# Optimization experiments

Hardware: AMD Instinct MI355X
Metric: run time of the kernel (lower is better)

The kernel has to match this reference:

```python
import jax, jax.numpy as jnp
import numpy as np

B, N, F_IN, F_OUT = 8, 4096, 256, 256


def setup_inputs() -> dict:
    key = jax.random.key(0)
    k1, k2, k3 = jax.random.split(key, 3)
    H = jax.random.normal(k1, (B, N, F_IN), dtype=jnp.float32)
    W = jax.random.normal(k2, (F_IN, F_OUT), dtype=jnp.float32) * (1.0 / np.sqrt(F_IN))
    A = jax.random.normal(k3, (N, N), dtype=jnp.float32) * (1.414 * np.sqrt(2.0 / (N + N)))
    return {"H": H, "W": W, "A": A}


def reference(H, W, A):
    # HW: [B, N, F_out]
    HW = jnp.einsum('bnf,fo->bno', H, W)
    # symmetrize + relu -> nonneg adjacency [N, N]
    A_norm = jax.nn.relu((A + A.T) * 0.5)
    # degree and inverse sqrt (inf -> 0 for isolated nodes)
    D = jnp.sum(A_norm, axis=1)
    D_safe = jnp.where(D > 0, D, 1.0)
    d_inv_sqrt = jnp.where(D > 0, D_safe ** -0.5, 0.0)
    # L_norm = I - D^{-1/2} A D^{-1/2}  (diagonal scaling, no dense diag matmul)
    DAD = d_inv_sqrt[:, None] * A_norm * d_inv_sqrt[None, :]
    L_norm = jnp.eye(N, dtype=H.dtype) - DAD
    # output = relu(L_norm @ HW): [B, N, F_out]
    out = jnp.einsum('nm,bmo->bno', L_norm, HW)
    return jax.nn.relu(out)
```

## Files before the change

### kernel.cpp

```cpp
#include <hip/hip_runtime.h>
#include <stdint.h>

#define N_NODES 4096
#define F_DIM   256
#define BATCH   8

typedef __attribute__((ext_vector_type(8))) __bf16 bf16x8;
typedef __attribute__((ext_vector_type(4))) float  f32x4;
typedef __attribute__((ext_vector_type(8))) unsigned short u16x8;

typedef const __attribute__((address_space(1))) void* gas1_t;
typedef __attribute__((address_space(3))) void*       las3_t;

__device__ __forceinline__ void stage16(const void* g, void* l) {
  __builtin_amdgcn_global_load_lds((gas1_t)g, (las3_t)l, 16, 0, 0);
}

__device__ __forceinline__ unsigned short f2bf(float f) {
  union { float f; uint32_t u; } v; v.f = f;
  uint32_t u = v.u;
  return (unsigned short)((u + 0x7FFFu + ((u >> 16) & 1u)) >> 16);
}
__device__ __forceinline__ float bf2f(unsigned short u) {
  union { uint32_t u; float f; } v; v.u = ((uint32_t)u) << 16;
  return v.f;
}

__global__ __launch_bounds__(256) void k_pre(const float* __restrict__ A,
                                             unsigned short* __restrict__ Sb,
                                             float* __restrict__ D,
                                             const float4* __restrict__ H4,
                                             ushort4* __restrict__ Hb4,
                                             const float* __restrict__ W,
                                             unsigned short* __restrict__ Wt) {
  int t = threadIdx.x;
  int bid = blockIdx.y * 64 + blockIdx.x;
  {
    int i = bid * 512 + t;
    float4 v = H4[i];
    ushort4 o; o.x = f2bf(v.x); o.y = f2bf(v.y); o.z = f2bf(v.z); o.w = f2bf(v.w);
    Hb4[i] = o;
    i += 256;
    v = H4[i];
    o.x = f2bf(v.x); o.y = f2bf(v.y); o.z = f2bf(v.z); o.w = f2bf(v.w);
    Hb4[i] = o;
  }
  if (bid < 256) Wt[t * 256 + bid] = f2bf(W[bid * 256 + t]);

  int bi = blockIdx.y, bj = blockIdx.x;
  if (bj < bi) return;

  __shared__ __align__(16) float T1[64][68];
  __shared__ float Tt[64][67];
  __shared__ float Pr4[64][4];
  __shared__ float Pc[4][64];
  int i0 = bi * 64, j0 = bj * 64;

#pragma unroll
  for (int it = 0; it < 4; ++it) {
    int idx = it * 256 + t;
    int r = idx >> 4, c4 = (idx & 15) * 4;
    float4 v1 = *(const float4*)(A + (size_t)(i0 + r) * N_NODES + j0 + c4);
    *(float4*)&T1[r][c4] = v1;
    float4 v2 = *(const float4*)(A + (size_t)(j0 + r) * N_NODES + i0 + c4);
    Tt[c4 + 0][r] = v2.x; Tt[c4 + 1][r] = v2.y; Tt[c4 + 2][r] = v2.z; Tt[c4 + 3][r] = v2.w;
  }
  __syncthreads();

  {
    int r = t >> 2, cb = (t & 3) * 8;
    float rowpart = 0.f;
#pragma unroll
    for (int g = 0; g < 2; ++g) {
      int c0 = cb + g * 32;
      u16x8 u;
      float vv[8];
#pragma unroll
      for (int i = 0; i < 8; ++i) {
        float v = 0.5f * (T1[r][c0 + i] + Tt[r][c0 + i]);
        v = v > 0.f ? v : 0.f;
        vv[i] = v;
        rowpart += v;
        u[i] = f2bf(v);
      }
      *(u16x8*)&Sb[(size_t)(i0 + r) * N_NODES + j0 + c0] = u;
      *(float4*)&T1[r][c0]     = make_float4(vv[0], vv[1], vv[2], vv[3]);
      *(float4*)&T1[r][c0 + 4] = make_float4(vv[4], vv[5], vv[6], vv[7]);
    }
    Pr4[r][t & 3] = rowpart;
  }
  __syncthreads();

  {
    int c = t & 63, seg = t >> 6;
    float s = 0.f;
#pragma unroll
    for (int i = 0; i < 16; ++i) s += T1[seg * 16 + i][c];
    Pc[seg][c] = s;
  }
  __syncthreads();

  if (t < 64) {
    atomicAdd(&D[i0 + t], Pr4[t][0] + Pr4[t][1] + Pr4[t][2] + Pr4[t][3]);
  } else if (t < 128 && bi != bj) {
    int c = t - 64;
    atomicAdd(&D[j0 + c], Pc[0][c] + Pc[1][c] + Pc[2][c] + Pc[3][c]);
  }

  if (bi != bj) {
#pragma unroll
    for (int it = 0; it < 2; ++it) {
      int u = it * 256 + t;
      int co = u >> 3, rc = (u & 7) * 8;
      u16x8 o;
#pragma unroll
      for (int i = 0; i < 8; ++i) o[i] = f2bf(T1[rc + i][co]);
      *(u16x8*)&Sb[(size_t)(j0 + co) * N_NODES + i0 + rc] = o;
    }
  }
}

__global__ void k_dinv(const float* __restrict__ D, float* __restrict__ dinv) {
  int i = blockIdx.x * blockDim.x + threadIdx.x;
  if (i < N_NODES) {
    float d = D[i];
    dinv[i] = d > 0.f ? 1.0f / sqrtf(d) : 0.f;
  }
}

__global__ __launch_bounds__(512) void k_gemm1(const unsigned short* __restrict__ Hb,
                                               const unsigned short* __restrict__ Wt,
                                               const float* __restrict__ dinv,
                                               unsigned short* __restrict__ HWb,
                                               unsigned short* __restrict__ Gt) {
  __shared__ __align__(16) unsigned short L[65536];
  int t = threadIdx.x;
  int lane = t & 63, r16 = lane & 15, q = lane >> 4;
  int wave = t >> 6;
  int wm = wave >> 2, wn = wave & 3;
  int nh = blockIdx.x;
  int m0 = blockIdx.y * 128;
  int n0 = nh * 128;

#pragma unroll
  for (int i = 0; i < 8; ++i) {
    int s = i * 512 + t;
    int row = s >> 5, cl = s & 31;
    int cs = cl ^ (row & 7);
    uint32_t dst = (uint32_t)(i * 512 + (t & ~63)) * 16;
    stage16(Hb + (size_t)(m0 + row) * 256 + cs * 8, (char*)L + dst);
    stage16(Wt + (size_t)(n0 + row) * 256 + cs * 8, (char*)L + 65536 + dst);
  }
  __syncthreads();

  f32x4 acc[4][2];
#pragma unroll
  for (int i = 0; i < 4; ++i)
#pragma unroll
    for (int j = 0; j < 2; ++j) acc[i][j] = f32x4{0.f, 0.f, 0.f, 0.f};

#pragma unroll
  for (int ks = 0; ks < 8; ++ks) {
    bf16x8 a[4], b[2];
#pragma unroll
    for (int mi = 0; mi < 4; ++mi) {
      int ra = wm * 64 + mi * 16 + r16;
      a[mi] = *(const bf16x8*)((const char*)L + ra * 512 + (((ks * 4 + q) ^ (ra & 7)) << 4));
    }
#pragma unroll
    for (int ni = 0; ni < 2; ++ni) {
      int rb = wn * 32 + ni * 16 + r16;
      b[ni] = *(const bf16x8*)((const char*)L + 65536 + rb * 512 + (((ks * 4 + q) ^ (rb & 7)) << 4));
    }
#pragma unroll
    for (int mi = 0; mi < 4; ++mi)
#pragma unroll
      for (int ni = 0; ni < 2; ++ni)
        acc[mi][ni] = __builtin_amdgcn_mfma_f32_16x16x32_bf16(a[mi], b[ni], acc[mi][ni], 0, 0, 0);
  }
  __syncthreads();

  unsigned short (*T)[136] = (unsigned short (*)[136])L;
#pragma unroll
  for (int mi = 0; mi < 4; ++mi) {
    int rowl = wm * 64 + mi * 16 + q * 4;
#pragma unroll
    for (int ni = 0; ni < 2; ++ni) {
      int coll = wn * 32 + ni * 16 + r16;
#pragma unroll
      for (int rr = 0; rr < 4; ++rr) {
        unsigned short h = f2bf(acc[mi][ni][rr]);
        HWb[(size_t)(m0 + rowl + rr) * F_DIM + (n0 + coll)] = h;
        T[coll][rowl + rr] = h;
      }
    }
  }
  __syncthreads();

  int b = m0 >> 12, nb = m0 & 4095;
#pragma unroll
  for (int i = 0; i < 4; ++i) {
    int u = i * 512 + t;
    int co = u >> 4, cs = (u & 15) * 8;
    u16x8 v = *(const u16x8*)&T[co][cs];
    float4 d0 = *(const float4*)&dinv[nb + cs];
    float4 d1 = *(const float4*)&dinv[nb + cs + 4];
    u16x8 w;
    w[0] = f2bf(bf2f(v[0]) * d0.x);
    w[1] = f2bf(bf2f(v[1]) * d0.y);
    w[2] = f2bf(bf2f(v[2]) * d0.z);
    w[3] = f2bf(bf2f(v[3]) * d0.w);
    w[4] = f2bf(bf2f(v[4]) * d1.x);
    w[5] = f2bf(bf2f(v[5]) * d1.y);
    w[6] = f2bf(bf2f(v[6]) * d1.z);
    w[7] = f2bf(bf2f(v[7]) * d1.w);
    *(u16x8*)&Gt[(size_t)(b * 256 + n0 + co) * N_NODES + nb + cs] = w;
  }
}

#define LDSB 49152

__global__ __launch_bounds__(512, 2) void k_gemm2(const unsigned short* __restrict__ Sb,
                                                  const unsigned short* __restrict__ Gt,
                                                  const unsigned short* __restrict__ HWb,
                                                  const float* __restrict__ dinv,
                                                  float* __restrict__ Out) {
  __shared__ __align__(16) unsigned short LDS[3 * 24576];
  const int NT = N_NODES / 64;
  int t = threadIdx.x;
  int lane = t & 63, r16 = lane & 15, q = lane >> 4;
  int wave = t >> 6;
  int wm = wave >> 1, wn = wave & 1;

  int bid = blockIdx.x;
  int xcd = bid & 7, j = bid >> 3;
  int mt = (xcd >> 1) * 4 + (j & 3);
  int nt = (xcd & 1) * 8 + (j >> 2);
  int m0 = mt * 256, n0 = nt * 128;

  const char* aSrc[4]; const char* bSrc[2];
  uint32_t aDst[4], bDst[2];
#pragma unroll
  for (int i = 0; i < 4; ++i) {
    int slot = i * 512 + t;
    int row = slot >> 3;
    int c = (slot & 7) ^ (row & 7);
    aSrc[i] = (const char*)Sb + (size_t)(m0 + row) * 8192 + c * 16;
    aDst[i] = (uint32_t)(i * 512 + (t & ~63)) * 16;
  }
#pragma unroll
  for (int i = 0; i < 2; ++i) {
    int slot = i * 512 + t;
    int row = slot >> 3;
    int c = (slot & 7) ^ (row & 7);
    bSrc[i] = (const char*)Gt + (size_t)(n0 + row) * 8192 + c * 16;
    bDst[i] = 32768u + (uint32_t)(i * 512 + (t & ~63)) * 16;
  }

  int aoff[4][2], boff[4][2];
#pragma unroll
  for (int mi = 0; mi < 4; ++mi) {
    int ra = wm * 64 + mi * 16 + r16;
#pragma unroll
    for (int ks = 0; ks < 2; ++ks)
      aoff[mi][ks] = ra * 128 + (((ks * 4 + q) ^ (ra & 7)) << 4);
  }
#pragma unroll
  for (int ni = 0; ni < 4; ++ni) {
    int rb = wn * 64 + ni * 16 + r16;
#pragma unroll
    for (int ks = 0; ks < 2; ++ks)
      boff[ni][ks] = 32768 + rb * 128 + (((ks * 4 + q) ^ (rb & 7)) << 4);
  }

  f32x4 acc[4][4];
#pragma unroll
  for (int i = 0; i < 4; ++i)
#pragma unroll
    for (int jj = 0; jj < 4; ++jj) acc[i][jj] = f32x4{0.f, 0.f, 0.f, 0.f};

  auto stage_tile = [&](int kt2, uint32_t bufByte) {
    size_t kb = (size_t)kt2 * 128;
#pragma unroll
    for (int i = 0; i < 4; ++i)
      stage16(aSrc[i] + kb, (char*)LDS + bufByte + aDst[i]);
#pragma unroll
    for (int i = 0; i < 2; ++i)
      stage16(bSrc[i] + kb, (char*)LDS + bufByte + bDst[i]);
  };

  auto tile_body = [&](int kt, uint32_t cur, int mode) {
    bf16x8 aR[4][2], bR[4][2];
#pragma unroll
    for (int mi = 0; mi < 4; ++mi)
#pragma unroll
      for (int ks = 0; ks < 2; ++ks)
        aR[mi][ks] = *(const bf16x8*)((const char*)LDS + cur + aoff[mi][ks]);
#pragma unroll
    for (int ni = 0; ni < 4; ++ni)
#pragma unroll
      for (int ks = 0; ks < 2; ++ks)
        bR[ni][ks] = *(const bf16x8*)((const char*)LDS + cur + boff[ni][ks]);
    if (mode == 2) {
      uint32_t stg = cur + 2 * LDSB;
      if (stg >= 3 * LDSB) stg -= 3 * LDSB;
      stage_tile(kt + 2, stg);
    }
    __builtin_amdgcn_sched_barrier(0);
    __builtin_amdgcn_s_setprio(1);
#pragma unroll
    for (int ks = 0; ks < 2; ++ks)
#pragma unroll
      for (int mi = 0; mi < 4; ++mi)
#pragma unroll
        for (int ni = 0; ni < 4; ++ni)
          acc[mi][ni] = __builtin_amdgcn_mfma_f32_16x16x32_bf16(aR[mi][ks], bR[ni][ks], acc[mi][ni], 0, 0, 0);
    __builtin_amdgcn_s_setprio(0);
    if (mode == 2) {
      asm volatile("s_waitcnt vmcnt(6)" ::: "memory");
    } else if (mode == 1) {
      asm volatile("s_waitcnt vmcnt(0)" ::: "memory");
    }
    if (mode != 0) {
      __builtin_amdgcn_s_barrier();
      __builtin_amdgcn_sched_barrier(0);
    }
  };

  stage_tile(0, 0);
  stage_tile(1, LDSB);
  asm volatile("s_waitcnt vmcnt(6)" ::: "memory");
  __builtin_amdgcn_s_barrier();
  __builtin_amdgcn_sched_barrier(0);

  uint32_t cur = 0;
#pragma unroll 1
  for (int kt = 0; kt < NT - 2; ++kt) {
    tile_body(kt, cur, 2);
    cur += LDSB; if (cur == 3 * LDSB) cur = 0;
  }
  tile_body(NT - 2, cur, 1);
  cur += LDSB; if (cur == 3 * LDSB) cur = 0;
  tile_body(NT - 1, cur, 0);

  int bq = n0 >> 8;
#pragma unroll
  for (int mi = 0; mi < 4; ++mi) {
    int row = m0 + wm * 64 + mi * 16 + q * 4;
    float di[4];
#pragma unroll
    for (int rr = 0; rr < 4; ++rr) di[rr] = dinv[row + rr];
#pragma unroll
    for (int ni = 0; ni < 4; ++ni) {
      int col = n0 + wn * 64 + ni * 16 + r16;
      int o = col & 255;
#pragma unroll
      for (int rr = 0; rr < 4; ++rr) {
        size_t oi = ((size_t)bq * N_NODES + (row + rr)) * F_DIM + o;
        float u = bf2f(HWb[oi]) - di[rr] * acc[mi][ni][rr];
        Out[oi] = u > 0.f ? u : 0.f;
      }
    }
  }
}

extern "C" void kernel_launch(void* const* d_in, const int* in_sizes, int n_in,
                              void* d_out, int out_size, void* d_ws, size_t ws_size,
                              hipStream_t stream) {
  (void)in_sizes; (void)n_in; (void)out_size; (void)ws_size;
  const float* H = (const float*)d_in[0];
  const float* W = (const float*)d_in[1];
  const float* A = (const float*)d_in[2];
  float* out = (float*)d_out;

  char* ws = (char*)d_ws;
  size_t off = 0;
  auto alloc = [&](size_t bytes) {
    char* p = ws + off;
    off += (bytes + 255) & ~(size_t)255;
    return p;
  };
  float*          Dd   = (float*)alloc((size_t)N_NODES * 4);
  float*          dinv = (float*)alloc((size_t)N_NODES * 4);
  unsigned short* Sb   = (unsigned short*)alloc((size_t)N_NODES * N_NODES * 2);
  unsigned short* HWb  = (unsigned short*)alloc((size_t)BATCH * N_NODES * F_DIM * 2);
  unsigned short* Gt   = (unsigned short*)alloc((size_t)BATCH * F_DIM * N_NODES * 2);
  unsigned short* Wt   = (unsigned short*)alloc((size_t)F_DIM * F_DIM * 2);
  unsigned short* Hb   = (unsigned short*)alloc((size_t)BATCH * N_NODES * F_DIM * 2);

  hipMemsetAsync(Dd, 0, N_NODES * 4, stream);
  k_pre<<<dim3(64, 64), 256, 0, stream>>>(A, Sb, Dd, (const float4*)H, (ushort4*)Hb, W, Wt);
  k_dinv<<<16, 256, 0, stream>>>(Dd, dinv);
  k_gemm1<<<dim3(2, 256), 512, 0, stream>>>(Hb, Wt, dinv, HWb, Gt);
  k_gemm2<<<dim3(256), 512, 0, stream>>>(Sb, Gt, HWb, dinv, out);
}
```

Measured before the change: 220.1 us.

## Pre-swizzle Gt into MFMA fragment layout and load B directly to registers

```diff
diff --git a/kernel.cpp b/kernel.cpp
--- a/kernel.cpp
+++ b/kernel.cpp
@@ -24,6 +24,9 @@
 __device__ __forceinline__ float bf2f(unsigned short u) {
   union { uint32_t u; float f; } v; v.u = ((uint32_t)u) << 16;
   return v.f;
+}
+__device__ __forceinline__ float dinv_of(float d) {
+  return d > 0.f ? 1.0f / sqrtf(d) : 0.f;
 }
 
 __global__ __launch_bounds__(256) void k_pre(const float* __restrict__ A,
@@ -67,28 +70,35 @@
   }
   __syncthreads();
 
-  {
-    int r = t >> 2, cb = (t & 3) * 8;
-    float rowpart = 0.f;
-#pragma unroll
-    for (int g = 0; g < 2; ++g) {
-      int c0 = cb + g * 32;
-      u16x8 u;
-      float vv[8];
-#pragma unroll
-      for (int i = 0; i < 8; ++i) {
-        float v = 0.5f * (T1[r][c0 + i] + Tt[r][c0 + i]);
-        v = v > 0.f ? v : 0.f;
-        vv[i] = v;
-        rowpart += v;
-        u[i] = f2bf(v);
-      }
-      *(u16x8*)&Sb[(size_t)(i0 + r) * N_NODES + j0 + c0] = u;
-      *(float4*)&T1[r][c0]     = make_float4(vv[0], vv[1], vv[2], vv[3]);
-      *(float4*)&T1[r][c0 + 4] = make_float4(vv[4], vv[5], vv[6], vv[7]);
-    }
-    Pr4[r][t & 3] = rowpart;
-  }
+  int r = t >> 2, cb = (t & 3) * 8;
+  float vv[16];
+  float rowpart = 0.f;
+#pragma unroll
+  for (int g = 0; g < 2; ++g) {
+    int c0 = cb + g * 32;
+#pragma unroll
+    for (int i = 0; i < 8; ++i) {
+      float v = 0.5f * (T1[r][c0 + i] + Tt[r][c0 + i]);
+      v = v > 0.f ? v : 0.f;
+      vv[g * 8 + i] = v;
+      rowpart += v;
+    }
+  }
+  __syncthreads();
+
+#pragma unroll
+  for (int g = 0; g < 2; ++g) {
+    int c0 = cb + g * 32;
+    u16x8 u;
+#pragma unroll
+    for (int i = 0; i < 8; ++i) u[i] = f2bf(vv[g * 8 + i]);
+    *(u16x8*)&Sb[(size_t)(i0 + r) * N_NODES + j0 + c0] = u;
+    *(float4*)&T1[r][c0]     = make_float4(vv[g*8+0], vv[g*8+1], vv[g*8+2], vv[g*8+3]);
+    *(float4*)&T1[r][c0 + 4] = make_float4(vv[g*8+4], vv[g*8+5], vv[g*8+6], vv[g*8+7]);
+#pragma unroll
+    for (int i = 0; i < 8; ++i) Tt[c0 + i][r] = vv[g * 8 + i];
+  }
+  Pr4[r][t & 3] = rowpart;
   __syncthreads();
 
   {
@@ -114,25 +124,17 @@
       int co = u >> 3, rc = (u & 7) * 8;
       u16x8 o;
 #pragma unroll
-      for (int i = 0; i < 8; ++i) o[i] = f2bf(T1[rc + i][co]);
+      for (int i = 0; i < 8; ++i) o[i] = f2bf(Tt[co][rc + i]);
       *(u16x8*)&Sb[(size_t)(j0 + co) * N_NODES + i0 + rc] = o;
     }
-  }
-}
-
-__global__ void k_dinv(const float* __restrict__ D, float* __restrict__ dinv) {
-  int i = blockIdx.x * blockDim.x + threadIdx.x;
-  if (i < N_NODES) {
-    float d = D[i];
-    dinv[i] = d > 0.f ? 1.0f / sqrtf(d) : 0.f;
   }
 }
 
 __global__ __launch_bounds__(512) void k_gemm1(const unsigned short* __restrict__ Hb,
                                                const unsigned short* __restrict__ Wt,
-                                               const float* __restrict__ dinv,
+                                               const float* __restrict__ D,
                                                unsigned short* __restrict__ HWb,
-                                               unsigned short* __restrict__ Gt) {
+                                               unsigned short* __restrict__ Gt2) {
   __shared__ __align__(16) unsigned short L[65536];
   int t = threadIdx.x;
   int lane = t & 63, r16 = lane & 15, q = lane >> 4;
@@ -203,30 +205,32 @@
     int u = i * 512 + t;
     int co = u >> 4, cs = (u & 15) * 8;
     u16x8 v = *(const u16x8*)&T[co][cs];
-    float4 d0 = *(const float4*)&dinv[nb + cs];
-    float4 d1 = *(const float4*)&dinv[nb + cs + 4];
+    float4 d0 = *(const float4*)&D[nb + cs];
+    float4 d1 = *(const float4*)&D[nb + cs + 4];
     u16x8 w;
-    w[0] = f2bf(bf2f(v[0]) * d0.x);
-    w[1] = f2bf(bf2f(v[1]) * d0.y);
-    w[2] = f2bf(bf2f(v[2]) * d0.z);
-    w[3] = f2bf(bf2f(v[3]) * d0.w);
-    w[4] = f2bf(bf2f(v[4]) * d1.x);
-    w[5] = f2bf(bf2f(v[5]) * d1.y);
-    w[6] = f2bf(bf2f(v[6]) * d1.z);
-    w[7] = f2bf(bf2f(v[7]) * d1.w);
-    *(u16x8*)&Gt[(size_t)(b * 256 + n0 + co) * N_NODES + nb + cs] = w;
-  }
-}
-
-#define LDSB 49152
+    w[0] = f2bf(bf2f(v[0]) * dinv_of(d0.x));
+    w[1] = f2bf(bf2f(v[1]) * dinv_of(d0.y));
+    w[2] = f2bf(bf2f(v[2]) * dinv_of(d0.z));
+    w[3] = f2bf(bf2f(v[3]) * dinv_of(d0.w));
+    w[4] = f2bf(bf2f(v[4]) * dinv_of(d1.x));
+    w[5] = f2bf(bf2f(v[5]) * dinv_of(d1.y));
+    w[6] = f2bf(bf2f(v[6]) * dinv_of(d1.z));
+    w[7] = f2bf(bf2f(v[7]) * dinv_of(d1.w));
+    int r_g = b * 256 + n0 + co;
+    int k   = nb + cs;
+    int rbg = r_g >> 4, rl = r_g & 15;
+    int ktv = k >> 6, ksv = (k >> 5) & 1, qv = (k >> 3) & 3;
+    size_t addr = ((((size_t)rbg * 64 + ktv) * 2 + ksv) * 64 + (qv * 16 + rl)) * 16;
+    *(u16x8*)((char*)Gt2 + addr) = w;
+  }
+}
 
 __global__ __launch_bounds__(512, 2) void k_gemm2(const unsigned short* __restrict__ Sb,
-                                                  const unsigned short* __restrict__ Gt,
+                                                  const unsigned short* __restrict__ Gt2,
                                                   const unsigned short* __restrict__ HWb,
-                                                  const float* __restrict__ dinv,
+                                                  const float* __restrict__ D,
                                                   float* __restrict__ Out) {
-  __shared__ __align__(16) unsigned short LDS[3 * 24576];
-  const int NT = N_NODES / 64;
+  __shared__ __align__(16) unsigned short LDS[3 * 16384];
   int t = threadIdx.x;
   int lane = t & 63, r16 = lane & 15, q = lane >> 4;
   int wave = t >> 6;
@@ -238,8 +242,8 @@
   int nt = (xcd & 1) * 8 + (j >> 2);
   int m0 = mt * 256, n0 = nt * 128;
 
-  const char* aSrc[4]; const char* bSrc[2];
-  uint32_t aDst[4], bDst[2];
+  const char* aSrc[4];
+  uint32_t aDst[4];
 #pragma unroll
   for (int i = 0; i < 4; ++i) {
     int slot = i * 512 + t;
@@ -248,16 +252,8 @@
     aSrc[i] = (const char*)Sb + (size_t)(m0 + row) * 8192 + c * 16;
     aDst[i] = (uint32_t)(i * 512 + (t & ~63)) * 16;
   }
-#pragma unroll
-  for (int i = 0; i < 2; ++i) {
-    int slot = i * 512 + t;
-    int row = slot >> 3;
-    int c = (slot & 7) ^ (row & 7);
-    bSrc[i] = (const char*)Gt + (size_t)(n0 + row) * 8192 + c * 16;
-    bDst[i] = 32768u + (uint32_t)(i * 512 + (t & ~63)) * 16;
-  }
-
-  int aoff[4][2], boff[4][2];
+
+  int aoff[4][2];
 #pragma unroll
   for (int mi = 0; mi < 4; ++mi) {
     int ra = wm * 64 + mi * 16 + r16;
@@ -265,12 +261,12 @@
     for (int ks = 0; ks < 2; ++ks)
       aoff[mi][ks] = ra * 128 + (((ks * 4 + q) ^ (ra & 7)) << 4);
   }
+
+  const char* bbase[4];
 #pragma unroll
   for (int ni = 0; ni < 4; ++ni) {
-    int rb = wn * 64 + ni * 16 + r16;
-#pragma unroll
-    for (int ks = 0; ks < 2; ++ks)
-      boff[ni][ks] = 32768 + rb * 128 + (((ks * 4 + q) ^ (rb & 7)) << 4);
+    int rbg = nt * 8 + wn * 4 + ni;
+    bbase[ni] = (const char*)Gt2 + (size_t)rbg * 131072 + lane * 16;
   }
 
   f32x4 acc[4][4];
@@ -278,35 +274,36 @@
   for (int i = 0; i < 4; ++i)
 #pragma unroll
     for (int jj = 0; jj < 4; ++jj) acc[i][jj] = f32x4{0.f, 0.f, 0.f, 0.f};
+
+  bf16x8 B0[4][2], B1[4][2];
 
   auto stage_tile = [&](int kt2, uint32_t bufByte) {
     size_t kb = (size_t)kt2 * 128;
 #pragma unroll
     for (int i = 0; i < 4; ++i)
       stage16(aSrc[i] + kb, (char*)LDS + bufByte + aDst[i]);
-#pragma unroll
-    for (int i = 0; i < 2; ++i)
-      stage16(bSrc[i] + kb, (char*)LDS + bufByte + bDst[i]);
   };
 
-  auto tile_body = [&](int kt, uint32_t cur, int mode) {
-    bf16x8 aR[4][2], bR[4][2];
+  auto body = [&](int kt, uint32_t cur, bf16x8 (&Bu)[4][2], bf16x8 (&Bl)[4][2], int mode) {
+    bf16x8 aR[4][2];
 #pragma unroll
     for (int mi = 0; mi < 4; ++mi)
 #pragma unroll
       for (int ks = 0; ks < 2; ++ks)
         aR[mi][ks] = *(const bf16x8*)((const char*)LDS + cur + aoff[mi][ks]);
-#pragma unroll
-    for (int ni = 0; ni < 4; ++ni)
-#pragma unroll
-      for (int ks = 0; ks < 2; ++ks)
-        bR[ni][ks] = *(const bf16x8*)((const char*)LDS + cur + boff[ni][ks]);
+    if (mode != 0) {
+      size_t ko = (size_t)(kt + 1) * 2048;
+#pragma unroll
+      for (int ni = 0; ni < 4; ++ni)
+#pragma unroll
+        for (int ks = 0; ks < 2; ++ks)
+          Bl[ni][ks] = *(const bf16x8*)(bbase[ni] + ko + ks * 1024);
+    }
     if (mode == 2) {
-      uint32_t stg = cur + 2 * LDSB;
-      if (stg >= 3 * LDSB) stg -= 3 * LDSB;
+      uint32_t stg = cur + 65536;
+      if (stg >= 98304) stg -= 98304;
       stage_tile(kt + 2, stg);
     }
-    __builtin_amdgcn_sched_barrier(0);
     __builtin_amdgcn_s_setprio(1);
 #pragma unroll
     for (int ks = 0; ks < 2; ++ks)
@@ -314,34 +311,41 @@
       for (int mi = 0; mi < 4; ++mi)
 #pragma unroll
         for (int ni = 0; ni < 4; ++ni)
-          acc[mi][ni] = __builtin_amdgcn_mfma_f32_16x16x32_bf16(aR[mi][ks], bR[ni][ks], acc[mi][ni], 0, 0, 0);
+          acc[mi][ni] = __builtin_amdgcn_mfma_f32_16x16x32_bf16(aR[mi][ks], Bu[ni][ks], acc[mi][ni], 0, 0, 0);
     __builtin_amdgcn_s_setprio(0);
     if (mode == 2) {
-      asm volatile("s_waitcnt vmcnt(6)" ::: "memory");
-    } else if (mode == 1) {
-      asm volatile("s_waitcnt vmcnt(0)" ::: "memory");
-    }
-    if (mode != 0) {
+      asm volatile("s_waitcnt vmcnt(12)" ::: "memory");
       __builtin_amdgcn_s_barrier();
       __builtin_amdgcn_sched_barrier(0);
+    } else if (mode == 1) {
+      asm volatile("s_waitcnt vmcnt(8)" ::: "memory");
+      __builtin_amdgcn_s_barrier();
+      __builtin_amdgcn_sched_barrier(0);
     }
   };
 
+#pragma unroll
+  for (int ni = 0; ni < 4; ++ni)
+#pragma unroll
+    for (int ks = 0; ks < 2; ++ks)
+      B0[ni][ks] = *(const bf16x8*)(bbase[ni] + ks * 1024);
   stage_tile(0, 0);
-  stage_tile(1, LDSB);
-  asm volatile("s_waitcnt vmcnt(6)" ::: "memory");
+  stage_tile(1, 32768);
+  asm volatile("s_waitcnt vmcnt(4)" ::: "memory");
   __builtin_amdgcn_s_barrier();
   __builtin_amdgcn_sched_barrier(0);
 
   uint32_t cur = 0;
 #pragma unroll 1
-  for (int kt = 0; kt < NT - 2; ++kt) {
-    tile_body(kt, cur, 2);
-    cur += LDSB; if (cur == 3 * LDSB) cur = 0;
-  }
-  tile_body(NT - 2, cur, 1);
-  cur += LDSB; if (cur == 3 * LDSB) cur = 0;
-  tile_body(NT - 1, cur, 0);
+  for (int kt = 0; kt < 62; kt += 2) {
+    body(kt, cur, B0, B1, 2);
+    cur += 32768; if (cur == 98304) cur = 0;
+    body(kt + 1, cur, B1, B0, 2);
+    cur += 32768; if (cur == 98304) cur = 0;
+  }
+  body(62, cur, B0, B1, 1);
+  cur += 32768; if (cur == 98304) cur = 0;
+  body(63, cur, B1, B0, 0);
 
   int bq = n0 >> 8;
 #pragma unroll
@@ -349,7 +353,7 @@
     int row = m0 + wm * 64 + mi * 16 + q * 4;
     float di[4];
 #pragma unroll
-    for (int rr = 0; rr < 4; ++rr) di[rr] = dinv[row + rr];
+    for (int rr = 0; rr < 4; ++rr) di[rr] = dinv_of(D[row + rr]);
 #pragma unroll
     for (int ni = 0; ni < 4; ++ni) {
       int col = n0 + wn * 64 + ni * 16 + r16;
@@ -381,16 +385,14 @@
     return p;
   };
   float*          Dd   = (float*)alloc((size_t)N_NODES * 4);
-  float*          dinv = (float*)alloc((size_t)N_NODES * 4);
   unsigned short* Sb   = (unsigned short*)alloc((size_t)N_NODES * N_NODES * 2);
   unsigned short* HWb  = (unsigned short*)alloc((size_t)BATCH * N_NODES * F_DIM * 2);
-  unsigned short* Gt   = (unsigned short*)alloc((size_t)BATCH * F_DIM * N_NODES * 2);
+  unsigned short* Gt2  = (unsigned short*)alloc((size_t)BATCH * F_DIM * N_NODES * 2);
   unsigned short* Wt   = (unsigned short*)alloc((size_t)F_DIM * F_DIM * 2);
   unsigned short* Hb   = (unsigned short*)alloc((size_t)BATCH * N_NODES * F_DIM * 2);
 
   hipMemsetAsync(Dd, 0, N_NODES * 4, stream);
   k_pre<<<dim3(64, 64), 256, 0, stream>>>(A, Sb, Dd, (const float4*)H, (ushort4*)Hb, W, Wt);
-  k_dinv<<<16, 256, 0, stream>>>(Dd, dinv);
-  k_gemm1<<<dim3(2, 256), 512, 0, stream>>>(Hb, Wt, dinv, HWb, Gt);
-  k_gemm2<<<dim3(256), 512, 0, stream>>>(Sb, Gt, HWb, dinv, out);
-}
+  k_gemm1<<<dim3(2, 256), 512, 0, stream>>>(Hb, Wt, Dd, HWb, Gt2);
+  k_gemm2<<<dim3(256), 512, 0, stream>>>(Sb, Gt2, HWb, Dd, out);
+}
```

Measured after the change: 243.3 us. +10.6%, slower.

## Replace atomic degree accumulation with separate row-sum kernel over bf16 adjacency

Applied to the files above, without the earlier changes.

```diff
diff --git a/kernel.cpp b/kernel.cpp
--- a/kernel.cpp
+++ b/kernel.cpp
@@ -25,10 +25,12 @@
   union { uint32_t u; float f; } v; v.u = ((uint32_t)u) << 16;
   return v.f;
 }
+__device__ __forceinline__ float dinv_of(float d) {
+  return d > 0.f ? 1.0f / sqrtf(d) : 0.f;
+}
 
 __global__ __launch_bounds__(256) void k_pre(const float* __restrict__ A,
                                              unsigned short* __restrict__ Sb,
-                                             float* __restrict__ D,
                                              const float4* __restrict__ H4,
                                              ushort4* __restrict__ Hb4,
                                              const float* __restrict__ W,
@@ -52,8 +54,6 @@
 
   __shared__ __align__(16) float T1[64][68];
   __shared__ float Tt[64][67];
-  __shared__ float Pr4[64][4];
-  __shared__ float Pc[4][64];
   int i0 = bi * 64, j0 = bj * 64;
 
 #pragma unroll
@@ -67,70 +67,68 @@
   }
   __syncthreads();
 
-  {
-    int r = t >> 2, cb = (t & 3) * 8;
-    float rowpart = 0.f;
+  int r = t >> 2, cb = (t & 3) * 8;
+  float vv[16];
+#pragma unroll
+  for (int g = 0; g < 2; ++g) {
+    int c0 = cb + g * 32;
+#pragma unroll
+    for (int i = 0; i < 8; ++i) {
+      float v = 0.5f * (T1[r][c0 + i] + Tt[r][c0 + i]);
+      vv[g * 8 + i] = v > 0.f ? v : 0.f;
+    }
+  }
+
+#pragma unroll
+  for (int g = 0; g < 2; ++g) {
+    int c0 = cb + g * 32;
+    u16x8 u;
+#pragma unroll
+    for (int i = 0; i < 8; ++i) u[i] = f2bf(vv[g * 8 + i]);
+    *(u16x8*)&Sb[(size_t)(i0 + r) * N_NODES + j0 + c0] = u;
+  }
+
+  if (bi != bj) {
+    __syncthreads();
 #pragma unroll
     for (int g = 0; g < 2; ++g) {
       int c0 = cb + g * 32;
-      u16x8 u;
-      float vv[8];
-#pragma unroll
-      for (int i = 0; i < 8; ++i) {
-        float v = 0.5f * (T1[r][c0 + i] + Tt[r][c0 + i]);
-        v = v > 0.f ? v : 0.f;
-        vv[i] = v;
-        rowpart += v;
-        u[i] = f2bf(v);
-      }
-      *(u16x8*)&Sb[(size_t)(i0 + r) * N_NODES + j0 + c0] = u;
-      *(float4*)&T1[r][c0]     = make_float4(vv[0], vv[1], vv[2], vv[3]);
-      *(float4*)&T1[r][c0 + 4] = make_float4(vv[4], vv[5], vv[6], vv[7]);
-    }
-    Pr4[r][t & 3] = rowpart;
-  }
-  __syncthreads();
-
-  {
-    int c = t & 63, seg = t >> 6;
-    float s = 0.f;
-#pragma unroll
-    for (int i = 0; i < 16; ++i) s += T1[seg * 16 + i][c];
-    Pc[seg][c] = s;
-  }
-  __syncthreads();
-
-  if (t < 64) {
-    atomicAdd(&D[i0 + t], Pr4[t][0] + Pr4[t][1] + Pr4[t][2] + Pr4[t][3]);
-  } else if (t < 128 && bi != bj) {
-    int c = t - 64;
-    atomicAdd(&D[j0 + c], Pc[0][c] + Pc[1][c] + Pc[2][c] + Pc[3][c]);
-  }
-
-  if (bi != bj) {
+#pragma unroll
+      for (int i = 0; i < 8; ++i) Tt[c0 + i][r] = vv[g * 8 + i];
+    }
+    __syncthreads();
 #pragma unroll
     for (int it = 0; it < 2; ++it) {
       int u = it * 256 + t;
       int co = u >> 3, rc = (u & 7) * 8;
       u16x8 o;
 #pragma unroll
-      for (int i = 0; i < 8; ++i) o[i] = f2bf(T1[rc + i][co]);
+      for (int i = 0; i < 8; ++i) o[i] = f2bf(Tt[co][rc + i]);
       *(u16x8*)&Sb[(size_t)(j0 + co) * N_NODES + i0 + rc] = o;
     }
   }
 }
 
-__global__ void k_dinv(const float* __restrict__ D, float* __restrict__ dinv) {
-  int i = blockIdx.x * blockDim.x + threadIdx.x;
-  if (i < N_NODES) {
-    float d = D[i];
-    dinv[i] = d > 0.f ? 1.0f / sqrtf(d) : 0.f;
-  }
+__global__ __launch_bounds__(256) void k_deg(const unsigned short* __restrict__ Sb,
+                                             float* __restrict__ D) {
+  int wave = threadIdx.x >> 6, lane = threadIdx.x & 63;
+  int row = blockIdx.x * 4 + wave;
+  const unsigned short* p = Sb + (size_t)row * N_NODES + lane * 8;
+  float s = 0.f;
+#pragma unroll
+  for (int i = 0; i < 8; ++i) {
+    u16x8 v = *(const u16x8*)(p + i * 512);
+#pragma unroll
+    for (int j = 0; j < 8; ++j) s += bf2f(v[j]);
+  }
+#pragma unroll
+  for (int off = 32; off >= 1; off >>= 1) s += __shfl_xor(s, off);
+  if (lane == 0) D[row] = s;
 }
 
 __global__ __launch_bounds__(512) void k_gemm1(const unsigned short* __restrict__ Hb,
                                                const unsigned short* __restrict__ Wt,
-                                               const float* __restrict__ dinv,
+                                               const float* __restrict__ D,
                                                unsigned short* __restrict__ HWb,
                                                unsigned short* __restrict__ Gt) {
   __shared__ __align__(16) unsigned short L[65536];
@@ -203,17 +201,17 @@
     int u = i * 512 + t;
     int co = u >> 4, cs = (u & 15) * 8;
     u16x8 v = *(const u16x8*)&T[co][cs];
-    float4 d0 = *(const float4*)&dinv[nb + cs];
-    float4 d1 = *(const float4*)&dinv[nb + cs + 4];
+    float4 d0 = *(const float4*)&D[nb + cs];
+    float4 d1 = *(const float4*)&D[nb + cs + 4];
     u16x8 w;
-    w[0] = f2bf(bf2f(v[0]) * d0.x);
-    w[1] = f2bf(bf2f(v[1]) * d0.y);
-    w[2] = f2bf(bf2f(v[2]) * d0.z);
-    w[3] = f2bf(bf2f(v[3]) * d0.w);
-    w[4] = f2bf(bf2f(v[4]) * d1.x);
-    w[5] = f2bf(bf2f(v[5]) * d1.y);
-    w[6] = f2bf(bf2f(v[6]) * d1.z);
-    w[7] = f2bf(bf2f(v[7]) * d1.w);
+    w[0] = f2bf(bf2f(v[0]) * dinv_of(d0.x));
+    w[1] = f2bf(bf2f(v[1]) * dinv_of(d0.y));
+    w[2] = f2bf(bf2f(v[2]) * dinv_of(d0.z));
+    w[3] = f2bf(bf2f(v[3]) * dinv_of(d0.w));
+    w[4] = f2bf(bf2f(v[4]) * dinv_of(d1.x));
+    w[5] = f2bf(bf2f(v[5]) * dinv_of(d1.y));
+    w[6] = f2bf(bf2f(v[6]) * dinv_of(d1.z));
+    w[7] = f2bf(bf2f(v[7]) * dinv_of(d1.w));
     *(u16x8*)&Gt[(size_t)(b * 256 + n0 + co) * N_NODES + nb + cs] = w;
   }
 }
@@ -223,7 +221,7 @@
 __global__ __launch_bounds__(512, 2) void k_gemm2(const unsigned short* __restrict__ Sb,
                                                   const unsigned short* __restrict__ Gt,
                                                   const unsigned short* __restrict__ HWb,
-                                                  const float* __restrict__ dinv,
+                                                  const float* __restrict__ D,
                                                   float* __restrict__ Out) {
   __shared__ __align__(16) unsigned short LDS[3 * 24576];
   const int NT = N_NODES / 64;
@@ -349,7 +347,7 @@
     int row = m0 + wm * 64 + mi * 16 + q * 4;
     float di[4];
 #pragma unroll
-    for (int rr = 0; rr < 4; ++rr) di[rr] = dinv[row + rr];
+    for (int rr = 0; rr < 4; ++rr) di[rr] = dinv_of(D[row + rr]);
 #pragma unroll
     for (int ni = 0; ni < 4; ++ni) {
       int col = n0 + wn * 64 + ni * 16 + r16;
@@ -381,16 +379,14 @@
     return p;
   };
   float*          Dd   = (float*)alloc((size_t)N_NODES * 4);
-  float*          dinv = (float*)alloc((size_t)N_NODES * 4);
   unsigned short* Sb   = (unsigned short*)alloc((size_t)N_NODES * N_NODES * 2);
   unsigned short* HWb  = (unsigned short*)alloc((size_t)BATCH * N_NODES * F_DIM * 2);
   unsigned short* Gt   = (unsigned short*)alloc((size_t)BATCH * F_DIM * N_NODES * 2);
   unsigned short* Wt   = (unsigned short*)alloc((size_t)F_DIM * F_DIM * 2);
   unsigned short* Hb   = (unsigned short*)alloc((size_t)BATCH * N_NODES * F_DIM * 2);
 
-  hipMemsetAsync(Dd, 0, N_NODES * 4, stream);
-  k_pre<<<dim3(64, 64), 256, 0, stream>>>(A, Sb, Dd, (const float4*)H, (ushort4*)Hb, W, Wt);
-  k_dinv<<<16, 256, 0, stream>>>(Dd, dinv);
-  k_gemm1<<<dim3(2, 256), 512, 0, stream>>>(Hb, Wt, dinv, HWb, Gt);
-  k_gemm2<<<dim3(256), 512, 0, stream>>>(Sb, Gt, HWb, dinv, out);
-}
+  k_pre<<<dim3(64, 64), 256, 0, stream>>>(A, Sb, (const float4*)H, (ushort4*)Hb, W, Wt);
+  k_deg<<<1024, 256, 0, stream>>>(Sb, Dd);
+  k_gemm1<<<dim3(2, 256), 512, 0, stream>>>(Hb, Wt, Dd, HWb, Gt);
+  k_gemm2<<<dim3(256), 512, 0, stream>>>(Sb, Gt, HWb, Dd, out);
+}
```

Measured after the change: 224.2 us. About the same (+1.8%).
